# Kernel optimization log

Measured on AMD Instinct MI355X. Metric: run time of the kernel, lower is better.

## Reference

```python
import jax, jax.numpy as jnp
import numpy as np

K = 3  # kernel_size


def setup_inputs() -> dict:
    key = jax.random.key(0)
    k1, k2, k3, k4, k5 = jax.random.split(key, 5)
    B, H, W, C, F = 8, 128, 128, 64, 128
    x_in = jax.random.normal(k1, (B, H, W, C), dtype=jnp.float32)
    # offset-predicting conv: k x k conv, C -> k*k channels (small init so offsets are moderate)
    offset_W = jax.random.normal(k2, (K, K, C, K * K), dtype=jnp.float32) * 0.05
    offset_b = jax.random.normal(k3, (K * K,), dtype=jnp.float32) * 0.05
    # main deformable conv weights: (k, k, C_in, F)
    conv_W = jax.random.normal(k4, (K, K, C, F), dtype=jnp.float32) * (1.0 / np.sqrt(K * K * C))
    conv_b = jax.random.normal(k5, (F,), dtype=jnp.float32) * 0.01
    return {"x_in": x_in, "offset_W": offset_W, "offset_b": offset_b,
            "conv_W": conv_W, "conv_b": conv_b}


def reference(x_in, offset_W, offset_b, conv_W, conv_b):
    B, H, W, C = x_in.shape
    k = offset_W.shape[0]
    pad = k // 2
    # 1) predict one scalar offset per output location per kernel tap
    offsets = jax.lax.conv_general_dilated(
        x_in, offset_W, window_strides=(1, 1), padding='SAME',
        dimension_numbers=('NHWC', 'HWIO', 'NHWC')) + offset_b  # (B,H,W,k*k)
    offsets = offsets.reshape(B, H, W, k, k)

    # 2) sampling grid: integer rows (clamped), fractional cols = base + offset
    i = jnp.arange(H)
    j = jnp.arange(W)
    p = jnp.arange(k) - pad
    q = jnp.arange(k) - pad
    yy = jnp.clip(i[:, None, None, None] + p[None, None, :, None], 0, H - 1)  # (H,1,k,1)
    yy = jnp.broadcast_to(yy, (H, W, k, k))
    xf = (j[None, :, None, None] + q[None, None, None, :]).astype(x_in.dtype) + offsets  # (B,H,W,k,k)
    x0 = jnp.floor(xf)
    w1 = xf - x0                                   # linear-interp weight, grads flow to offsets
    x0i = jnp.clip(x0.astype(jnp.int32), 0, W - 1)
    x1i = jnp.clip(x0i + 1, 0, W - 1)

    # 3) bilinear (1-D linear) gather per batch element
    def sample(xb, x0b, x1b, wb):
        s0 = xb[yy, x0b]  # (H,W,k,k,C)
        s1 = xb[yy, x1b]
        return s0 * (1.0 - wb[..., None]) + s1 * wb[..., None]

    sampled = jax.vmap(sample)(x_in, x0i, x1i, w1)  # (B,H,W,k,k,C)

    # 4) weighted convolution sum over taps and input channels
    out = jnp.einsum('bijpqc,pqcf->bijf', sampled, conv_W) + conv_b  # (B,H,W,F)
    return out
```

## Files before the change

### kernel.cpp

```cpp
#include <hip/hip_runtime.h>
#include <hip/hip_bf16.h>


typedef __attribute__((ext_vector_type(8))) short short8;
typedef __attribute__((ext_vector_type(4))) float f32x4;

#define CWB_BYTES (18 * 4 * 128 * 8 * 2)
#define OFFS_OFF  CWB_BYTES
#define OFFS_BYTES (131072 * 9 * 4)
#define WS_SPLIT  (CWB_BYTES + OFFS_BYTES)

__device__ __forceinline__ unsigned short f2bf(float f) {
  union { float f; unsigned u; } v; v.f = f;
  unsigned r = v.u + 0x7fffu + ((v.u >> 16) & 1u);
  return (unsigned short)(r >> 16);
}

__device__ __forceinline__ unsigned pk2bf(float a, float b) {
  __hip_bfloat162 h = __float22bfloat162_rn(make_float2(a, b));
  union { __hip_bfloat162 h; unsigned u; } c; c.h = h;
  return c.u;
}

__global__ __launch_bounds__(256) void offsets_pack_kernel(
    const float* __restrict__ x, const float* __restrict__ oW,
    const float* __restrict__ ob, const float* __restrict__ cW,
    float* __restrict__ offs, unsigned short* __restrict__ cWb) {
  const int hw = blockIdx.x;
  if (hw >= 512) {
    const int t = (hw - 512) * 256 + threadIdx.x;
    if (t < 73728) {
      const int k = t >> 7, f = t & 127;
      const int ks = k >> 5, q4 = (k >> 3) & 3, jj = k & 7;
      cWb[(size_t)(((ks * 4 + q4) * 128 + f) * 8 + jj)] = f2bf(cW[t]);
    }
    return;
  }
  const int logical = ((hw & 7) << 6) | (hw >> 3);
  const int pix = logical * 256 + threadIdx.x;
  const int j = pix & 127;
  const int i = (pix >> 7) & 127;
  const int b = pix >> 14;
  float acc[9];
#pragma unroll
  for (int t = 0; t < 9; ++t) acc[t] = ob[t];
  const float* xb = x + ((size_t)b << 20);
#pragma unroll
  for (int p = 0; p < 3; ++p) {
    const int yy = i + p - 1;
    if (yy < 0 || yy > 127) continue;
#pragma unroll
    for (int q = 0; q < 3; ++q) {
      const int xx = j + q - 1;
      if (xx < 0 || xx > 127) continue;
      const float4* xp = (const float4*)(xb + (((yy << 7) + xx) << 6));
      float4 v[16];
#pragma unroll
      for (int c4 = 0; c4 < 16; ++c4) v[c4] = xp[c4];
      const float* wp = oW + (p * 3 + q) * 576;
#pragma unroll
      for (int c4 = 0; c4 < 16; ++c4) {
        const float* w = wp + c4 * 36;
#pragma unroll
        for (int t = 0; t < 9; ++t) acc[t] += v[c4].x * w[t];
#pragma unroll
        for (int t = 0; t < 9; ++t) acc[t] += v[c4].y * w[9 + t];
#pragma unroll
        for (int t = 0; t < 9; ++t) acc[t] += v[c4].z * w[18 + t];
#pragma unroll
        for (int t = 0; t < 9; ++t) acc[t] += v[c4].w * w[27 + t];
      }
    }
  }
  float* op = offs + (size_t)pix * 9;
#pragma unroll
  for (int t = 0; t < 9; ++t) op[t] = acc[t];
}

__global__ __launch_bounds__(512, 2) void main_kernel(
    const float* __restrict__ x, const float* __restrict__ offs,
    const float* __restrict__ cb, float* __restrict__ out,
    const unsigned short* __restrict__ cWb) {
  __shared__ __align__(16) char lds[64 * 576 * 2];
  __shared__ float offw[576];
  __shared__ int2 gmeta[576];

  const int tid = threadIdx.x;
  const int hwbid = blockIdx.x;
  const int bid = ((hwbid & 7) << 8) | (hwbid >> 3);
  const int j0 = (bid & 1) << 6;
  const int i = (bid >> 1) & 127;
  const int b = bid >> 8;
  const float* xb = x + ((size_t)b << 20);

  const int lane = tid & 63;
  const int wv = tid >> 6;

  const size_t base9 = ((size_t)(((b << 7) | i) << 7) | j0) * 9;
  for (int item = tid; item < 576; item += 512) {
    const int pix = item / 9;
    const int tap = item - pix * 9;
    const float off = offs[base9 + item];
    const int p = tap / 3;
    const int q = tap - p * 3;
    int yy = i + p - 1;
    yy = yy < 0 ? 0 : (yy > 127 ? 127 : yy);
    const float xf = (float)(j0 + pix + q - 1) + off;
    const float x0f = floorf(xf);
    const float w1 = xf - x0f;
    int x0i = (int)x0f;
    x0i = x0i < 0 ? 0 : (x0i > 127 ? 127 : x0i);
    const int x1i = (x0i + 1 > 127) ? 127 : x0i + 1;
    gmeta[item].x = ((yy << 7) + x0i) << 8;
    gmeta[item].y = ((yy << 7) + x1i) << 8;
    offw[item] = w1;
  }
  __syncthreads();

#pragma unroll
  for (int batch = 0; batch < 6; ++batch) {
    int a0_[3], a1_[3], sb[3];
    float sw1[3];
#pragma unroll
    for (int s = 0; s < 3; ++s) {
      const int idx = tid + (batch * 3 + s) * 512;
      const int c4 = idx & 15;
      const int pair = idx >> 4;
      const int2 g = gmeta[pair];
      sw1[s] = offw[pair];
      a0_[s] = g.x + (c4 << 4);
      a1_[s] = g.y + (c4 << 4);
      const int pix8 = (pair / 9) & 7;
      sb[s] = ((pair << 7) + (c4 << 3)) ^ (pix8 << 4);
    }
    float4 s0[3], s1[3];
#pragma unroll
    for (int s = 0; s < 3; ++s) {
      s0[s] = *(const float4*)((const char*)xb + a0_[s]);
      s1[s] = *(const float4*)((const char*)xb + a1_[s]);
    }
    asm volatile("" :: "v"(s0[0].x), "v"(s0[1].x), "v"(s0[2].x),
                       "v"(s1[0].x), "v"(s1[1].x), "v"(s1[2].x));
    __builtin_amdgcn_sched_barrier(0);
#pragma unroll
    for (int s = 0; s < 3; ++s) {
      const float w1 = sw1[s];
      uint2 pk;
      pk.x = pk2bf(s0[s].x + w1 * (s1[s].x - s0[s].x),
                   s0[s].y + w1 * (s1[s].y - s0[s].y));
      pk.y = pk2bf(s0[s].z + w1 * (s1[s].z - s0[s].z),
                   s0[s].w + w1 * (s1[s].w - s0[s].w));
      *(uint2*)(lds + sb[s]) = pk;
    }
  }
  __syncthreads();

  const int f0 = (wv >> 1) << 5;
  const int colf = lane & 15;
  const int q4 = lane >> 4;
  const int pixr0 = ((wv & 1) << 4) + colf;
  f32x4 a00 = {0.f, 0.f, 0.f, 0.f}, a01 = a00, a10 = a00, a11 = a00;
  short8 bf0, bf1;
  {
    const unsigned short* wb = cWb + (size_t)((q4 * 128 + f0 + colf) * 8);
    bf0 = *(const short8*)wb;
    bf1 = *(const short8*)(wb + 128);
  }
  for (int ks = 0; ks < 18; ++ks) {
    const int aoff = (pixr0 * 1152 + ks * 64 + q4 * 16) ^ ((pixr0 & 7) << 4);
    const short8 af0 = *(const short8*)(lds + aoff);
    const short8 af1 = *(const short8*)(lds + aoff + 32 * 1152);
    short8 nb0, nb1;
    if (ks < 17) {
      const unsigned short* wn =
          cWb + (size_t)((((ks + 1) * 4 + q4) * 128 + f0 + colf) * 8);
      nb0 = *(const short8*)wn;
      nb1 = *(const short8*)(wn + 128);
    }
    a00 = __builtin_amdgcn_mfma_f32_16x16x32_bf16(bf0, af0, a00, 0, 0, 0);
    a01 = __builtin_amdgcn_mfma_f32_16x16x32_bf16(bf1, af0, a01, 0, 0, 0);
    a10 = __builtin_amdgcn_mfma_f32_16x16x32_bf16(bf0, af1, a10, 0, 0, 0);
    a11 = __builtin_amdgcn_mfma_f32_16x16x32_bf16(bf1, af1, a11, 0, 0, 0);
    if (ks < 17) { bf0 = nb0; bf1 = nb1; }
  }
  __syncthreads();

  float* const outS = (float*)lds;
  {
    const float4 cb0 = *(const float4*)(cb + f0 + q4 * 4);
    const float4 cb1 = *(const float4*)(cb + f0 + 16 + q4 * 4);
    float4 r;
    r.x = a00[0] + cb0.x; r.y = a00[1] + cb0.y;
    r.z = a00[2] + cb0.z; r.w = a00[3] + cb0.w;
    *(float4*)(outS + pixr0 * 132 + f0 + q4 * 4) = r;
    r.x = a01[0] + cb1.x; r.y = a01[1] + cb1.y;
    r.z = a01[2] + cb1.z; r.w = a01[3] + cb1.w;
    *(float4*)(outS + pixr0 * 132 + f0 + 16 + q4 * 4) = r;
    r.x = a10[0] + cb0.x; r.y = a10[1] + cb0.y;
    r.z = a10[2] + cb0.z; r.w = a10[3] + cb0.w;
    *(float4*)(outS + (pixr0 + 32) * 132 + f0 + q4 * 4) = r;
    r.x = a11[0] + cb1.x; r.y = a11[1] + cb1.y;
    r.z = a11[2] + cb1.z; r.w = a11[3] + cb1.w;
    *(float4*)(outS + (pixr0 + 32) * 132 + f0 + 16 + q4 * 4) = r;
  }
  __syncthreads();
  float4* og = (float4*)(out + (((size_t)((b << 14) | (i << 7) | j0)) << 7));
#pragma unroll
  for (int r = 0; r < 4; ++r) {
    const int f4i = r * 512 + tid;
    const int pp = f4i >> 5, ff = f4i & 31;
    og[pp * 32 + ff] = *(const float4*)(outS + pp * 132 + ff * 4);
  }
}

__global__ __launch_bounds__(512, 8) void fused_deform_kernel(
    const float* __restrict__ x, const float* __restrict__ oW,
    const float* __restrict__ ob, const float* __restrict__ cW,
    const float* __restrict__ cb, float* __restrict__ out) {
  __shared__ __align__(16) char lds[32 * 576 * 2];
  __shared__ float offs_s[288];
  float* const xtile = (float*)lds;

  const int tid = threadIdx.x;
  const int bid = blockIdx.x;
  const int j0 = (bid & 3) << 5;
  const int i = (bid >> 2) & 127;
  const int b = bid >> 9;
  const float* xb = x + ((size_t)b << 20);
  const int lane = tid & 63;
  const int wv = tid >> 6;

  for (int t = tid; t < 3 * 34 * 16; t += 512) {
    const int c4 = t & 15;
    const int cc = (t >> 4) % 34;
    const int r = (t >> 4) / 34;
    const int row = i + r - 1;
    const int col = j0 + cc - 1;
    float4 v = make_float4(0.f, 0.f, 0.f, 0.f);
    if (row >= 0 && row <= 127 && col >= 0 && col <= 127)
      v = ((const float4*)(xb + (((row << 7) + col) << 6)))[c4];
    *(float4*)(xtile + (r * 34 + cc) * 68 + c4 * 4) = v;
  }
  __syncthreads();

  for (int t = tid; t < 576; t += 512) {
    const int half = t & 1;
    const int item = t >> 1;
    const int ochan = item % 9;
    const int pix = item / 9;
    const int c4base = half << 3;
    f32x4 acc = {0.f, 0.f, 0.f, 0.f};
#pragma unroll
    for (int pq = 0; pq < 9; ++pq) {
      const int p = pq / 3, q = pq - p * 3;
      const float4* xr = (const float4*)(xtile + (p * 34 + pix + q) * 68) + c4base;
      const float* wr = oW + (size_t)(pq * 64 + c4base * 4) * 9 + ochan;
#pragma unroll
      for (int c4 = 0; c4 < 8; ++c4) {
        const float4 v = xr[c4];
        acc.x += v.x * wr[(c4 * 4 + 0) * 9];
        acc.y += v.y * wr[(c4 * 4 + 1) * 9];
        acc.z += v.z * wr[(c4 * 4 + 2) * 9];
        acc.w += v.w * wr[(c4 * 4 + 3) * 9];
      }
    }
    float s = (acc.x + acc.y) + (acc.z + acc.w);
    s += __shfl_xor(s, 1);
    if (!half) offs_s[item] = s + ob[ochan];
  }
  __syncthreads();

  for (int it = tid; it < 32 * 9 * 16; it += 512) {
    const int c4 = it & 15;
    const int tmp = it >> 4;
    const int tap = tmp % 9;
    const int pix = tmp / 9;
    const int j = j0 + pix;
    const float off = offs_s[pix * 9 + tap];
    const int p = tap / 3;
    const int q = tap - p * 3;
    int yy = i + p - 1;
    yy = yy < 0 ? 0 : (yy > 127 ? 127 : yy);
    const float xf = (float)(j + q - 1) + off;
    const float x0f = floorf(xf);
    const float w1 = xf - x0f;
    int x0i = (int)x0f;
    x0i = x0i < 0 ? 0 : (x0i > 127 ? 127 : x0i);
    const int x1i = (x0i + 1 > 127) ? 127 : x0i + 1;
    const float4 s0 = ((const float4*)(xb + (((yy << 7) + x0i) << 6)))[c4];
    const float4 s1 = ((const float4*)(xb + (((yy << 7) + x1i) << 6)))[c4];
    const float w0 = 1.0f - w1;
    const int boff = (pix * 1152 + tap * 128 + c4 * 8) ^ ((pix & 7) << 4);
    uint2 pk;
    pk.x = (unsigned)f2bf(s0.x * w0 + s1.x * w1) |
           ((unsigned)f2bf(s0.y * w0 + s1.y * w1) << 16);
    pk.y = (unsigned)f2bf(s0.z * w0 + s1.z * w1) |
           ((unsigned)f2bf(s0.w * w0 + s1.w * w1) << 16);
    *(uint2*)(lds + boff) = pk;
  }
  __syncthreads();

  const int m = wv & 1;
  const int f0 = (wv >> 1) << 5;
  const int colf = lane & 15;
  const int q4 = lane >> 4;
  const int pixr = m * 16 + colf;
  f32x4 a0 = {0.f, 0.f, 0.f, 0.f}, a1 = a0;
  for (int ks = 0; ks < 18; ++ks) {
    const int aoff = (pixr * 1152 + ks * 64 + q4 * 16) ^ ((pixr & 7) << 4);
    const short8 af = *(const short8*)(lds + aoff);
    short8 bf0, bf1;
    const float* wp = cW + (size_t)(ks * 32 + q4 * 8) * 128 + f0 + colf;
#pragma unroll
    for (int jj = 0; jj < 8; ++jj) bf0[jj] = (short)f2bf(wp[jj * 128]);
#pragma unroll
    for (int jj = 0; jj < 8; ++jj) bf1[jj] = (short)f2bf(wp[jj * 128 + 16]);
    a0 = __builtin_amdgcn_mfma_f32_16x16x32_bf16(bf0, af, a0, 0, 0, 0);
    a1 = __builtin_amdgcn_mfma_f32_16x16x32_bf16(bf1, af, a1, 0, 0, 0);
  }

  const float cb0s = cb[f0 + colf];
  const float cb1s = cb[f0 + 16 + colf];
  float* obase = out + (((size_t)((b << 14) | (i << 7) | j0)) << 7);
#pragma unroll
  for (int reg = 0; reg < 4; ++reg) {
    float* r = obase + (size_t)(m * 16 + q4 * 4 + reg) * 128;
    r[f0 + colf] = a0[reg] + cb0s;
    r[f0 + 16 + colf] = a1[reg] + cb1s;
  }
}

extern "C" void kernel_launch(void* const* d_in, const int* in_sizes, int n_in,
                              void* d_out, int out_size, void* d_ws, size_t ws_size,
                              hipStream_t stream) {
  const float* x = (const float*)d_in[0];
  const float* oW = (const float*)d_in[1];
  const float* ob = (const float*)d_in[2];
  const float* cW = (const float*)d_in[3];
  const float* cb = (const float*)d_in[4];
  float* out = (float*)d_out;

  if (ws_size >= WS_SPLIT) {
    unsigned short* cWb = (unsigned short*)d_ws;
    float* offs = (float*)((char*)d_ws + OFFS_OFF);
    hipLaunchKernelGGL(offsets_pack_kernel, dim3(800), dim3(256), 0, stream,
                       x, oW, ob, cW, offs, cWb);
    hipLaunchKernelGGL(main_kernel, dim3(2048), dim3(512), 0, stream,
                       x, offs, cb, out, cWb);
  } else {
    hipLaunchKernelGGL(fused_deform_kernel, dim3(4096), dim3(512), 0, stream,
                       x, oW, ob, cW, cb, out);
  }
}
```

Measured before the change: 103.0 us.

## Split offset conv across 16 lanes per pixel with LDS weights and shuffle reduce

The offset-predicting conv used to run one thread per pixel, with 64-channel float4 loads per tap and weights read from global memory. It now gives each pixel 16 threads, one per float4 channel group, so x loads coalesce. Transposed offset weights are staged in LDS and the per-thread partial sums are reduced with xor shuffles. The weight packing moves into its own kernel, which adds a launch and extra workspace for the transposed offset weights.

```diff
diff --git a/kernel.cpp b/kernel.cpp
--- a/kernel.cpp
+++ b/kernel.cpp
@@ -5,10 +5,12 @@
 typedef __attribute__((ext_vector_type(8))) short short8;
 typedef __attribute__((ext_vector_type(4))) float f32x4;
 
-#define CWB_BYTES (18 * 4 * 128 * 8 * 2)
-#define OFFS_OFF  CWB_BYTES
+#define CWB_BYTES  (18 * 4 * 128 * 8 * 2)
+#define OWT_OFF    CWB_BYTES
+#define OWT_BYTES  (9 * 9 * 64 * 4)
+#define OFFS_OFF   (OWT_OFF + OWT_BYTES)
 #define OFFS_BYTES (131072 * 9 * 4)
-#define WS_SPLIT  (CWB_BYTES + OFFS_BYTES)
+#define WS_SPLIT   (OFFS_OFF + OFFS_BYTES)
 
 __device__ __forceinline__ unsigned short f2bf(float f) {
   union { float f; unsigned u; } v; v.f = f;
@@ -22,29 +24,46 @@
   return c.u;
 }
 
-__global__ __launch_bounds__(256) void offsets_pack_kernel(
-    const float* __restrict__ x, const float* __restrict__ oW,
-    const float* __restrict__ ob, const float* __restrict__ cW,
-    float* __restrict__ offs, unsigned short* __restrict__ cWb) {
+__global__ __launch_bounds__(256) void pack_kernel(
+    const float* __restrict__ cW, const float* __restrict__ oW,
+    unsigned short* __restrict__ cWb, float* __restrict__ oWt) {
+  const int t = blockIdx.x * 256 + threadIdx.x;
+  if (t < 73728) {
+    const int k = t >> 7, f = t & 127;
+    const int ks = k >> 5, q4 = (k >> 3) & 3, jj = k & 7;
+    cWb[(size_t)(((ks * 4 + q4) * 128 + f) * 8 + jj)] = f2bf(cW[t]);
+  }
+  if (t < 5184) {
+    const int pq = t / 576;
+    const int r = t - pq * 576;
+    const int tt = r >> 6;
+    const int ch = r & 63;
+    oWt[t] = oW[(size_t)(pq * 64 + ch) * 9 + tt];
+  }
+}
+
+__global__ __launch_bounds__(256) void offsets_kernel(
+    const float* __restrict__ x, const float* __restrict__ oWt,
+    const float* __restrict__ ob, float* __restrict__ offs) {
+  __shared__ __align__(16) float wL[81 * 64];
+  const int tid = threadIdx.x;
+  for (int it = tid; it < 1296; it += 256)
+    ((float4*)wL)[it] = ((const float4*)oWt)[it];
+  __syncthreads();
+
   const int hw = blockIdx.x;
-  if (hw >= 512) {
-    const int t = (hw - 512) * 256 + threadIdx.x;
-    if (t < 73728) {
-      const int k = t >> 7, f = t & 127;
-      const int ks = k >> 5, q4 = (k >> 3) & 3, jj = k & 7;
-      cWb[(size_t)(((ks * 4 + q4) * 128 + f) * 8 + jj)] = f2bf(cW[t]);
-    }
-    return;
-  }
-  const int logical = ((hw & 7) << 6) | (hw >> 3);
-  const int pix = logical * 256 + threadIdx.x;
-  const int j = pix & 127;
-  const int i = (pix >> 7) & 127;
-  const int b = pix >> 14;
+  const int logical = ((hw & 7) << 10) | (hw >> 3);
+  const int gpix = logical * 16 + (tid >> 4);
+  const int c4 = tid & 15;
+  const int j = gpix & 127;
+  const int i = (gpix >> 7) & 127;
+  const int b = gpix >> 14;
+  const float* xb = x + ((size_t)b << 20);
+
   float acc[9];
 #pragma unroll
-  for (int t = 0; t < 9; ++t) acc[t] = ob[t];
-  const float* xb = x + ((size_t)b << 20);
+  for (int t = 0; t < 9; ++t) acc[t] = 0.f;
+
 #pragma unroll
   for (int p = 0; p < 3; ++p) {
     const int yy = i + p - 1;
@@ -53,28 +72,27 @@
     for (int q = 0; q < 3; ++q) {
       const int xx = j + q - 1;
       if (xx < 0 || xx > 127) continue;
-      const float4* xp = (const float4*)(xb + (((yy << 7) + xx) << 6));
-      float4 v[16];
-#pragma unroll
-      for (int c4 = 0; c4 < 16; ++c4) v[c4] = xp[c4];
-      const float* wp = oW + (p * 3 + q) * 576;
-#pragma unroll
-      for (int c4 = 0; c4 < 16; ++c4) {
-        const float* w = wp + c4 * 36;
-#pragma unroll
-        for (int t = 0; t < 9; ++t) acc[t] += v[c4].x * w[t];
-#pragma unroll
-        for (int t = 0; t < 9; ++t) acc[t] += v[c4].y * w[9 + t];
-#pragma unroll
-        for (int t = 0; t < 9; ++t) acc[t] += v[c4].z * w[18 + t];
-#pragma unroll
-        for (int t = 0; t < 9; ++t) acc[t] += v[c4].w * w[27 + t];
+      const float4 v = ((const float4*)(xb + (((yy << 7) + xx) << 6)))[c4];
+      const float4* wrow = (const float4*)wL + (p * 3 + q) * 9 * 16 + c4;
+#pragma unroll
+      for (int t = 0; t < 9; ++t) {
+        const float4 w4 = wrow[t * 16];
+        acc[t] += v.x * w4.x + v.y * w4.y + v.z * w4.z + v.w * w4.w;
       }
     }
   }
-  float* op = offs + (size_t)pix * 9;
-#pragma unroll
-  for (int t = 0; t < 9; ++t) op[t] = acc[t];
+#pragma unroll
+  for (int t = 0; t < 9; ++t) {
+    acc[t] += __shfl_xor(acc[t], 1);
+    acc[t] += __shfl_xor(acc[t], 2);
+    acc[t] += __shfl_xor(acc[t], 4);
+    acc[t] += __shfl_xor(acc[t], 8);
+  }
+  if (c4 == 0) {
+    float* op = offs + (size_t)gpix * 9;
+#pragma unroll
+    for (int t = 0; t < 9; ++t) op[t] = acc[t] + ob[t];
+  }
 }
 
 __global__ __launch_bounds__(512, 2) void main_kernel(
@@ -342,9 +360,12 @@
 
   if (ws_size >= WS_SPLIT) {
     unsigned short* cWb = (unsigned short*)d_ws;
+    float* oWt = (float*)((char*)d_ws + OWT_OFF);
     float* offs = (float*)((char*)d_ws + OFFS_OFF);
-    hipLaunchKernelGGL(offsets_pack_kernel, dim3(800), dim3(256), 0, stream,
-                       x, oW, ob, cW, offs, cWb);
+    hipLaunchKernelGGL(pack_kernel, dim3(288), dim3(256), 0, stream,
+                       cW, oW, cWb, oWt);
+    hipLaunchKernelGGL(offsets_kernel, dim3(8192), dim3(256), 0, stream,
+                       x, oWt, ob, offs);
     hipLaunchKernelGGL(main_kernel, dim3(2048), dim3(512), 0, stream,
                        x, offs, cb, out, cWb);
   } else {
```

Measured after the change: 95.47 us. 1.08x faster.
